# Optimization experiments

Hardware: AMD Instinct MI355X
Metric: run time of the kernel (lower is better)

The kernel has to match this reference:

```python
import jax, jax.numpy as jnp
import numpy as np
from jax import lax

CH = 16      # channel_n
HID = 128    # hidden_n
WDIM = 128   # w_dim


def _sobel_weight():
    sx = np.array([[-1, 0, 1], [-2, 0, 2], [-1, 0, 1]], dtype=np.float32).reshape(1, 1, 3, 3)
    sy = np.array([[-1, -2, -1], [0, 0, 0], [1, 2, 1]], dtype=np.float32).reshape(1, 1, 3, 3)
    sx = np.repeat(sx, CH, axis=0)  # [16,1,3,3]
    sy = np.repeat(sy, CH, axis=0)  # [16,1,3,3]
    return jnp.asarray(np.concatenate([sx, sy], axis=0))  # [32,1,3,3] torch grouped-conv OIHW layout


def setup_inputs() -> dict:
    key = jax.random.key(0)
    k1, k2, k3, k4 = jax.random.split(key, 4)
    B, H, W = 8, 96, 96
    x = jax.random.uniform(k1, (B, CH, H, W), dtype=jnp.float32)
    w = jax.random.normal(k2, (B, WDIM), dtype=jnp.float32)
    sobel = _sobel_weight()
    # update_net params. NOTE: original fills W2 with 0.0 (trivial delta); we use
    W1 = jax.random.normal(k3, (HID, 3 * CH + WDIM), dtype=jnp.float32) * 0.05
    b1 = jnp.zeros((HID,), dtype=jnp.float32)
    W2 = jax.random.normal(k4, (CH, HID), dtype=jnp.float32) * 0.02
    return {"x": x, "w": w, "sobel": sobel, "W1": W1, "b1": b1, "W2": W2, "steps": 64}


def _living_mask(alpha):
    # max_pool2d(3, stride=1, pad=1) > 0.1 ; torch pads with -inf for max pool
    m = lax.reduce_window(alpha, -jnp.inf, lax.max, (1, 1, 3, 3), (1, 1, 1, 1), 'SAME')
    return m > 0.1


def reference(x, w, sobel, W1, b1, W2, steps):
    B, _, H, Wd = x.shape
    w_exp = jnp.broadcast_to(w[:, :, None, None], (B, WDIM, H, Wd))

    def step(xc, key):
        pre_life = _living_mask(xc[:, 3:4])
        perception = lax.conv_general_dilated(
            xc, sobel, (1, 1), 'SAME', feature_group_count=CH,
            dimension_numbers=('NCHW', 'OIHW', 'NCHW'))  # [B,32,H,W]
        comb = jnp.concatenate([xc, perception, w_exp], axis=1)  # [B,176,H,W]
        h = jax.nn.relu(jnp.einsum('bchw,nc->bnhw', comb, W1) + b1[None, :, None, None])
        delta = jnp.einsum('bnhw,cn->bchw', h, W2)
        alpha = xc[:, 3:4]
        upd = (jax.random.uniform(key, alpha.shape) < 0.5) & (alpha > 0.1)
        xn = xc + delta * upd.astype(xc.dtype)
        life = pre_life & _living_mask(xn[:, 3:4])
        xn = xn * life.astype(xn.dtype)
        return xn, None

    keys = jax.random.split(jax.random.key(42), steps)
    x_final, _ = lax.scan(step, x, keys)
    return x_final
```

## Files before the change

kernel.cpp:

```cpp
#include <hip/hip_runtime.h>
#include <stdint.h>


#define CHN 16
#define HIDN 128
#define WD 128
#define NB 8
#define NH 96
#define NW 96
#define NSTEPS 64
#define TW 16
#define TH 4
#define PLANE (NH*NW)
#define TILES_X (NW/TW)
#define TILES_Y (NH/TH)
#define TPI (TILES_X*TILES_Y)
#define NBLK (NB*TPI)
#define HW_ (TH+2)
#define WW_ (TW+2)
#define NF4 (HW_*WW_*4)
#define NT 256

typedef float v2f __attribute__((ext_vector_type(2)));

__host__ __device__ __forceinline__ uint32_t rotl(uint32_t v, int d){ return (v<<d)|(v>>(32-d)); }

__host__ __device__ __forceinline__ void threefry2x32(uint32_t k0, uint32_t k1,
                                                      uint32_t x0, uint32_t x1,
                                                      uint32_t &o0, uint32_t &o1){
  uint32_t k2 = k0 ^ k1 ^ 0x1BD11BDAu;
  x0 += k0; x1 += k1;
  x0 += x1; x1 = rotl(x1,13); x1 ^= x0;
  x0 += x1; x1 = rotl(x1,15); x1 ^= x0;
  x0 += x1; x1 = rotl(x1,26); x1 ^= x0;
  x0 += x1; x1 = rotl(x1, 6); x1 ^= x0;
  x0 += k1; x1 += k2 + 1u;
  x0 += x1; x1 = rotl(x1,17); x1 ^= x0;
  x0 += x1; x1 = rotl(x1,29); x1 ^= x0;
  x0 += x1; x1 = rotl(x1,16); x1 ^= x0;
  x0 += x1; x1 = rotl(x1,24); x1 ^= x0;
  x0 += k2; x1 += k0 + 2u;
  x0 += x1; x1 = rotl(x1,13); x1 ^= x0;
  x0 += x1; x1 = rotl(x1,15); x1 ^= x0;
  x0 += x1; x1 = rotl(x1,26); x1 ^= x0;
  x0 += x1; x1 = rotl(x1, 6); x1 ^= x0;
  x0 += k0; x1 += k1 + 3u;
  x0 += x1; x1 = rotl(x1,17); x1 ^= x0;
  x0 += x1; x1 = rotl(x1,29); x1 ^= x0;
  x0 += x1; x1 = rotl(x1,16); x1 ^= x0;
  x0 += x1; x1 = rotl(x1,24); x1 ^= x0;
  x0 += k1; x1 += k2 + 4u;
  x0 += x1; x1 = rotl(x1,13); x1 ^= x0;
  x0 += x1; x1 = rotl(x1,15); x1 ^= x0;
  x0 += x1; x1 = rotl(x1,26); x1 ^= x0;
  x0 += x1; x1 = rotl(x1, 6); x1 ^= x0;
  x0 += k2; x1 += k0 + 5u;
  o0 = x0; o1 = x1;
}

__global__ __launch_bounds__(256) void nca_pre(
    const float* __restrict__ w, const float* __restrict__ W1,
    const float* __restrict__ b1, const float* __restrict__ W2,
    float* __restrict__ w1eff, float* __restrict__ w2t, float* __restrict__ c1)
{
  const int b = blockIdx.x, t = threadIdx.x;
  if (b == 0){
    for (int idx = t; idx < HIDN*32; idx += 256){
      int n = idx >> 5, k = idx & 31;
      float v;
      if (k < 16) v = W1[n*176 + k];
      else { int cc = k - 16; v = W1[n*176 + 16 + 2*cc] + W1[n*176 + 17 + 2*cc]; }
      w1eff[idx] = v;
    }
    for (int idx = t; idx < HIDN*CHN; idx += 256){
      int n = idx >> 4, cc = idx & 15;
      w2t[idx] = W2[cc*HIDN + n];
    }
  }
  if (t < HIDN){
    float s = b1[t];
    const float* wrow = W1 + t*176 + 48;
    const float* wb = w + b*WD;
    #pragma unroll 8
    for (int k = 0; k < WD; ++k) s = fmaf(wrow[k], wb[k], s);
    c1[b*HIDN + t] = s;
  }
}

template<bool FIRST>
__global__ __launch_bounds__(NT, 4) void nca_step(
    const float* __restrict__ Xin,
    const unsigned char* __restrict__ Mp,
    const float* __restrict__ w1eff, const float* __restrict__ w2t,
    const float* __restrict__ c1,
    uint32_t key0, uint32_t key1,
    float* __restrict__ Yn, unsigned char* __restrict__ Mn)
{
  __shared__ float xs[HW_][WW_][20];
  __shared__ float ya[TH+4][TW+4];
  __shared__ float lifes[HW_][WW_];
  __shared__ float ufs[64];
  __shared__ float red[4][CHN][64];

  const int T = blockIdx.x;
  const int b = T & 7;
  const int t = T >> 3;
  const int tw0 = (t % TILES_X)*TW, th0 = (t / TILES_X)*TH;
  const int tid = threadIdx.x;

  if (FIRST){
    for (int idx = tid; idx < CHN*HW_*WW_; idx += NT){
      int ch = idx / (HW_*WW_), rem = idx % (HW_*WW_);
      int hh = rem / WW_, ww = rem % WW_;
      int g2 = th0 - 1 + hh, w2 = tw0 - 1 + ww;
      float v = 0.f;
      if ((unsigned)g2 < NH && (unsigned)w2 < NW)
        v = Xin[((b*CHN + ch)*NH + g2)*NW + w2];
      xs[hh][ww][ch] = v;
    }
  } else {
    if (tid < (TH+4)*(TW+4)){
      int hh = tid / (TW+4), ww = tid % (TW+4);
      int g2 = th0 - 2 + hh, w2 = tw0 - 2 + ww;
      float v = 0.f;
      if ((unsigned)g2 < NH && (unsigned)w2 < NW)
        v = Xin[(size_t)(b*PLANE + g2*NW + w2)*CHN + 3];
      ya[hh][ww] = v;
    }
    float4 xr[2];
    #pragma unroll
    for (int i = 0; i < 2; ++i){
      int idx = tid + i*NT;
      float4 v = make_float4(0.f,0.f,0.f,0.f);
      if (idx < NF4){
        int hh = idx / (WW_*4);
        int rem = idx % (WW_*4);
        int ww = rem >> 2, k4 = rem & 3;
        int g2 = th0 - 1 + hh, w2 = tw0 - 1 + ww;
        if ((unsigned)g2 < NH && (unsigned)w2 < NW)
          v = *(const float4*)(Xin + (size_t)(b*PLANE + g2*NW + w2)*CHN + k4*4);
      }
      xr[i] = v;
    }
    __syncthreads();
    if (tid < HW_*WW_){
      int hh = tid / WW_, ww = tid % WW_;
      int g2 = th0 - 1 + hh, w2 = tw0 - 1 + ww;
      float lf = 0.f;
      if ((unsigned)g2 < NH && (unsigned)w2 < NW){
        float mx = ya[hh][ww];
        #pragma unroll
        for (int dr = 0; dr < 3; ++dr)
          #pragma unroll
          for (int dc = 0; dc < 3; ++dc)
            mx = fmaxf(mx, ya[hh+dr][ww+dc]);
        lf = (Mp[b*PLANE + g2*NW + w2] && (mx > 0.1f)) ? 1.f : 0.f;
      }
      lifes[hh][ww] = lf;
    }
    __syncthreads();
    #pragma unroll
    for (int i = 0; i < 2; ++i){
      int idx = tid + i*NT;
      if (idx < NF4){
        int hh = idx / (WW_*4);
        int rem = idx % (WW_*4);
        int ww = rem >> 2, k4 = rem & 3;
        float lf = lifes[hh][ww];
        float4 v = xr[i];
        v.x *= lf; v.y *= lf; v.z *= lf; v.w *= lf;
        *(float4*)&xs[hh][ww][k4*4] = v;
      }
    }
  }
  __syncthreads();

  const int px = tid & 63;
  const int q  = tid >> 6;
  const int c = px & 15, r = px >> 4;
  const int gh = th0 + r, gw = tw0 + c;
  const int pos = b*PLANE + gh*NW + gw;

  #define LD4(dr,dc,k4) (*(const float4*)&xs[r+(dr)][c+(dc)][(k4)*4])
  const v2f two = (v2f){2.f, 2.f};
  float4 xc4[4];
  v2f xp[8], pp[8];
  #pragma unroll
  for (int k4 = 0; k4 < 4; ++k4){
    xc4[k4] = LD4(1,1,k4);
    xp[2*k4]   = (v2f){xc4[k4].x, xc4[k4].y};
    xp[2*k4+1] = (v2f){xc4[k4].z, xc4[k4].w};
  }
  #pragma unroll
  for (int k4 = 0; k4 < 2; ++k4){
    float4 a = LD4(0,2,k4), b0 = LD4(0,0,k4);
    float4 d = LD4(1,2,k4), e = LD4(1,0,k4);
    float4 f = LD4(2,2,k4), g = LD4(2,0,k4);
    v2f a0 = (v2f){a.x,a.y}, a1 = (v2f){a.z,a.w};
    v2f b0v= (v2f){b0.x,b0.y},b1v= (v2f){b0.z,b0.w};
    v2f d0 = (v2f){d.x,d.y}, d1 = (v2f){d.z,d.w};
    v2f e0 = (v2f){e.x,e.y}, e1 = (v2f){e.z,e.w};
    v2f f0 = (v2f){f.x,f.y}, f1 = (v2f){f.z,f.w};
    v2f g0 = (v2f){g.x,g.y}, g1 = (v2f){g.z,g.w};
    pp[2*k4]   = (a0-b0v) + two*(d0-e0) + (f0-g0);
    pp[2*k4+1] = (a1-b1v) + two*(d1-e1) + (f1-g1);
  }
  #pragma unroll
  for (int k4 = 2; k4 < 4; ++k4){
    float4 a = LD4(2,0,k4), b0 = LD4(0,0,k4);
    float4 d = LD4(2,1,k4), e = LD4(0,1,k4);
    float4 f = LD4(2,2,k4), g = LD4(0,2,k4);
    v2f a0 = (v2f){a.x,a.y}, a1 = (v2f){a.z,a.w};
    v2f b0v= (v2f){b0.x,b0.y},b1v= (v2f){b0.z,b0.w};
    v2f d0 = (v2f){d.x,d.y}, d1 = (v2f){d.z,d.w};
    v2f e0 = (v2f){e.x,e.y}, e1 = (v2f){e.z,e.w};
    v2f f0 = (v2f){f.x,f.y}, f1 = (v2f){f.z,f.w};
    v2f g0 = (v2f){g.x,g.y}, g1 = (v2f){g.z,g.w};
    pp[2*k4]   = (a0-b0v) + two*(d0-e0) + (f0-g0);
    pp[2*k4+1] = (a1-b1v) + two*(d1-e1) + (f1-g1);
  }
  #undef LD4

  if (q == 0){
    uint32_t o0, o1;
    threefry2x32(key0, key1, 0u, (uint32_t)pos, o0, o1);
    ufs[px] = ((((o0 ^ o1) >> 31) == 0u) && (xc4[0].w > 0.1f)) ? 1.f : 0.f;
  } else if (q == 1){
    float mx = xs[r][c][3];
    #pragma unroll
    for (int dr = 0; dr < 3; ++dr)
      #pragma unroll
      for (int dc = 0; dc < 3; ++dc)
        mx = fmaxf(mx, xs[r+dr][c+dc][3]);
    Mn[pos] = (mx > 0.1f) ? (unsigned char)1 : (unsigned char)0;
  }

  v2f acc2[8];
  #pragma unroll
  for (int i = 0; i < 8; ++i) acc2[i] = (v2f){0.f, 0.f};
  const int nbase = __builtin_amdgcn_readfirstlane(q) << 5;
  const float* c1b = c1 + b*HIDN;

  #pragma unroll 4
  for (int nn = 0; nn < 32; ++nn){
    const int n = nbase + nn;
    const v2f* wx = (const v2f*)(w1eff + (n << 5));
    v2f h01 = (v2f){c1b[n], 0.f};
    v2f h23 = (v2f){0.f, 0.f};
    #pragma unroll
    for (int k = 0; k < 8; ++k){
      h01 = __builtin_elementwise_fma(xp[k], wx[k],   h01);
      h23 = __builtin_elementwise_fma(pp[k], wx[8+k], h23);
    }
    float hv = fmaxf((h01.x + h01.y) + (h23.x + h23.y), 0.f);
    v2f hvv = (v2f){hv, hv};
    const v2f* w2p = (const v2f*)(w2t + (n << 4));
    #pragma unroll
    for (int cc2 = 0; cc2 < 8; ++cc2)
      acc2[cc2] = __builtin_elementwise_fma(hvv, w2p[cc2], acc2[cc2]);
  }

  #pragma unroll
  for (int cc2 = 0; cc2 < 8; ++cc2){
    red[q][2*cc2  ][px] = acc2[cc2].x;
    red[q][2*cc2+1][px] = acc2[cc2].y;
  }
  __syncthreads();

  {
    float uf = ufs[px];
    int ch = q << 2;
    float v0 = ((red[0][ch+0][px] + red[1][ch+0][px]) + (red[2][ch+0][px] + red[3][ch+0][px]));
    float v1 = ((red[0][ch+1][px] + red[1][ch+1][px]) + (red[2][ch+1][px] + red[3][ch+1][px]));
    float v2 = ((red[0][ch+2][px] + red[1][ch+2][px]) + (red[2][ch+2][px] + red[3][ch+2][px]));
    float v3 = ((red[0][ch+3][px] + red[1][ch+3][px]) + (red[2][ch+3][px] + red[3][ch+3][px]));
    float4 o = make_float4(fmaf(v0, uf, xc4[q].x), fmaf(v1, uf, xc4[q].y),
                           fmaf(v2, uf, xc4[q].z), fmaf(v3, uf, xc4[q].w));
    *(float4*)(Yn + (size_t)pos*CHN + q*4) = o;
  }
}

__global__ __launch_bounds__(256) void nca_final(
    const float* __restrict__ Yp, const unsigned char* __restrict__ Mp,
    float* __restrict__ out)
{
  __shared__ float ya[TH+4][TW+4];
  __shared__ float lifes[TH][TW];
  const int T = blockIdx.x;
  const int b = T & 7;
  const int t = T >> 3;
  const int tw0 = (t % TILES_X)*TW, th0 = (t / TILES_X)*TH;
  const int tid = threadIdx.x;
  if (tid < (TH+4)*(TW+4)){
    int hh = tid / (TW+4), ww = tid % (TW+4);
    int g2 = th0 - 2 + hh, w2 = tw0 - 2 + ww;
    float v = 0.f;
    if ((unsigned)g2 < NH && (unsigned)w2 < NW)
      v = Yp[(size_t)(b*PLANE + g2*NW + w2)*CHN + 3];
    ya[hh][ww] = v;
  }
  __syncthreads();
  if (tid < TH*TW){
    int i = tid >> 4, j = tid & 15;
    float mx = ya[i+2][j+2];
    #pragma unroll
    for (int dr = 0; dr < 3; ++dr)
      #pragma unroll
      for (int dc = 0; dc < 3; ++dc)
        mx = fmaxf(mx, ya[i+1+dr][j+1+dc]);
    lifes[i][j] = (Mp[b*PLANE + (th0+i)*NW + (tw0+j)] && (mx > 0.1f)) ? 1.f : 0.f;
  }
  __syncthreads();
  for (int idx = tid; idx < CHN*TH*TW; idx += 256){
    int ch = idx >> 6, p = idx & 63;
    int i = p >> 4, j = p & 15;
    int pos = b*PLANE + (th0+i)*NW + (tw0+j);
    out[((b*CHN + ch)*NH + th0 + i)*NW + tw0 + j] = Yp[(size_t)pos*CHN + ch] * lifes[i][j];
  }
}

extern "C" void kernel_launch(void* const* d_in, const int* in_sizes, int n_in,
                              void* d_out, int out_size, void* d_ws, size_t ws_size,
                              hipStream_t stream) {
  const float* x  = (const float*)d_in[0];
  const float* w  = (const float*)d_in[1];
  const float* W1 = (const float*)d_in[3];
  const float* b1 = (const float*)d_in[4];
  const float* W2 = (const float*)d_in[5];
  float* out = (float*)d_out;
  char* ws = (char*)d_ws;

  size_t off = 0;
  float*    w1eff = (float*)(ws + off);    off += (size_t)HIDN*32*4;
  float*    w2t   = (float*)(ws + off);    off += (size_t)HIDN*CHN*4;
  float*    c1    = (float*)(ws + off);    off += (size_t)NB*HIDN*4;
  float*    Yb0   = (float*)(ws + off);    off += (size_t)NB*CHN*PLANE*4;
  float*    Yb1   = (float*)(ws + off);    off += (size_t)NB*CHN*PLANE*4;
  unsigned char* Mb0 = (unsigned char*)(ws + off); off += (size_t)NB*PLANE;
  unsigned char* Mb1 = (unsigned char*)(ws + off); off += (size_t)NB*PLANE;
  (void)ws_size; (void)in_sizes; (void)n_in; (void)out_size;

  uint32_t k0[NSTEPS], k1[NSTEPS];
  for (int s = 0; s < NSTEPS; ++s) threefry2x32(0u, 42u, 0u, (uint32_t)s, k0[s], k1[s]);

  nca_pre<<<dim3(NB), dim3(256), 0, stream>>>(w, W1, b1, W2, w1eff, w2t, c1);

  nca_step<true><<<dim3(NBLK), dim3(NT), 0, stream>>>(
      x, Mb1 , w1eff, w2t, c1, k0[0], k1[0], Yb0, Mb0);
  for (int s = 1; s < NSTEPS; ++s){
    const float* Yp = (s & 1) ? Yb0 : Yb1;
    float*       Yn = (s & 1) ? Yb1 : Yb0;
    const unsigned char* Mq = (s & 1) ? Mb0 : Mb1;
    unsigned char*       Mn = (s & 1) ? Mb1 : Mb0;
    nca_step<false><<<dim3(NBLK), dim3(NT), 0, stream>>>(
        Yp, Mq, w1eff, w2t, c1, k0[s], k1[s], Yn, Mn);
  }
  nca_final<<<dim3(NBLK), dim3(256), 0, stream>>>(Yb1, Mb1, out);
}
```

Measured before the change: 1.391 ms.

## Double tile height so each thread computes two pixels sharing weight loads

```diff
diff --git a/kernel.cpp b/kernel.cpp
--- a/kernel.cpp
+++ b/kernel.cpp
@@ -10,7 +10,7 @@
 #define NW 96
 #define NSTEPS 64
 #define TW 16
-#define TH 4
+#define TH 8
 #define PLANE (NH*NW)
 #define TILES_X (NW/TW)
 #define TILES_Y (NH/TH)
@@ -87,8 +87,49 @@
   }
 }
 
+__device__ __forceinline__ void perceive_nhwc(const float xs[HW_][WW_][20],
+                                              int r, int c, v2f* xp, v2f* pp){
+  #define LD4(dr,dc,k4) (*(const float4*)&xs[r+(dr)][c+(dc)][(k4)*4])
+  const v2f two = (v2f){2.f, 2.f};
+  #pragma unroll
+  for (int k4 = 0; k4 < 4; ++k4){
+    float4 v = LD4(1,1,k4);
+    xp[2*k4]   = (v2f){v.x, v.y};
+    xp[2*k4+1] = (v2f){v.z, v.w};
+  }
+  #pragma unroll
+  for (int k4 = 0; k4 < 2; ++k4){
+    float4 a = LD4(0,2,k4), b0 = LD4(0,0,k4);
+    float4 d = LD4(1,2,k4), e = LD4(1,0,k4);
+    float4 f = LD4(2,2,k4), g = LD4(2,0,k4);
+    v2f a0 = (v2f){a.x,a.y}, a1 = (v2f){a.z,a.w};
+    v2f b0v= (v2f){b0.x,b0.y},b1v= (v2f){b0.z,b0.w};
+    v2f d0 = (v2f){d.x,d.y}, d1 = (v2f){d.z,d.w};
+    v2f e0 = (v2f){e.x,e.y}, e1 = (v2f){e.z,e.w};
+    v2f f0 = (v2f){f.x,f.y}, f1 = (v2f){f.z,f.w};
+    v2f g0 = (v2f){g.x,g.y}, g1 = (v2f){g.z,g.w};
+    pp[2*k4]   = (a0-b0v) + two*(d0-e0) + (f0-g0);
+    pp[2*k4+1] = (a1-b1v) + two*(d1-e1) + (f1-g1);
+  }
+  #pragma unroll
+  for (int k4 = 2; k4 < 4; ++k4){
+    float4 a = LD4(2,0,k4), b0 = LD4(0,0,k4);
+    float4 d = LD4(2,1,k4), e = LD4(0,1,k4);
+    float4 f = LD4(2,2,k4), g = LD4(0,2,k4);
+    v2f a0 = (v2f){a.x,a.y}, a1 = (v2f){a.z,a.w};
+    v2f b0v= (v2f){b0.x,b0.y},b1v= (v2f){b0.z,b0.w};
+    v2f d0 = (v2f){d.x,d.y}, d1 = (v2f){d.z,d.w};
+    v2f e0 = (v2f){e.x,e.y}, e1 = (v2f){e.z,e.w};
+    v2f f0 = (v2f){f.x,f.y}, f1 = (v2f){f.z,f.w};
+    v2f g0 = (v2f){g.x,g.y}, g1 = (v2f){g.z,g.w};
+    pp[2*k4]   = (a0-b0v) + two*(d0-e0) + (f0-g0);
+    pp[2*k4+1] = (a1-b1v) + two*(d1-e1) + (f1-g1);
+  }
+  #undef LD4
+}
+
 template<bool FIRST>
-__global__ __launch_bounds__(NT, 4) void nca_step(
+__global__ __launch_bounds__(NT, 3) void nca_step(
     const float* __restrict__ Xin,
     const unsigned char* __restrict__ Mp,
     const float* __restrict__ w1eff, const float* __restrict__ w2t,
@@ -99,8 +140,8 @@
   __shared__ float xs[HW_][WW_][20];
   __shared__ float ya[TH+4][TW+4];
   __shared__ float lifes[HW_][WW_];
-  __shared__ float ufs[64];
-  __shared__ float red[4][CHN][64];
+  __shared__ float ufs[128];
+  __shared__ float red[4][CHN][128];
 
   const int T = blockIdx.x;
   const int b = T & 7;
@@ -127,9 +168,9 @@
         v = Xin[(size_t)(b*PLANE + g2*NW + w2)*CHN + 3];
       ya[hh][ww] = v;
     }
-    float4 xr[2];
-    #pragma unroll
-    for (int i = 0; i < 2; ++i){
+    float4 xr[3];
+    #pragma unroll
+    for (int i = 0; i < 3; ++i){
       int idx = tid + i*NT;
       float4 v = make_float4(0.f,0.f,0.f,0.f);
       if (idx < NF4){
@@ -160,7 +201,7 @@
     }
     __syncthreads();
     #pragma unroll
-    for (int i = 0; i < 2; ++i){
+    for (int i = 0; i < 3; ++i){
       int idx = tid + i*NT;
       if (idx < NF4){
         int hh = idx / (WW_*4);
@@ -177,67 +218,44 @@
 
   const int px = tid & 63;
   const int q  = tid >> 6;
-  const int c = px & 15, r = px >> 4;
-  const int gh = th0 + r, gw = tw0 + c;
-  const int pos = b*PLANE + gh*NW + gw;
-
-  #define LD4(dr,dc,k4) (*(const float4*)&xs[r+(dr)][c+(dc)][(k4)*4])
-  const v2f two = (v2f){2.f, 2.f};
-  float4 xc4[4];
-  v2f xp[8], pp[8];
-  #pragma unroll
-  for (int k4 = 0; k4 < 4; ++k4){
-    xc4[k4] = LD4(1,1,k4);
-    xp[2*k4]   = (v2f){xc4[k4].x, xc4[k4].y};
-    xp[2*k4+1] = (v2f){xc4[k4].z, xc4[k4].w};
-  }
-  #pragma unroll
-  for (int k4 = 0; k4 < 2; ++k4){
-    float4 a = LD4(0,2,k4), b0 = LD4(0,0,k4);
-    float4 d = LD4(1,2,k4), e = LD4(1,0,k4);
-    float4 f = LD4(2,2,k4), g = LD4(2,0,k4);
-    v2f a0 = (v2f){a.x,a.y}, a1 = (v2f){a.z,a.w};
-    v2f b0v= (v2f){b0.x,b0.y},b1v= (v2f){b0.z,b0.w};
-    v2f d0 = (v2f){d.x,d.y}, d1 = (v2f){d.z,d.w};
-    v2f e0 = (v2f){e.x,e.y}, e1 = (v2f){e.z,e.w};
-    v2f f0 = (v2f){f.x,f.y}, f1 = (v2f){f.z,f.w};
-    v2f g0 = (v2f){g.x,g.y}, g1 = (v2f){g.z,g.w};
-    pp[2*k4]   = (a0-b0v) + two*(d0-e0) + (f0-g0);
-    pp[2*k4+1] = (a1-b1v) + two*(d1-e1) + (f1-g1);
-  }
-  #pragma unroll
-  for (int k4 = 2; k4 < 4; ++k4){
-    float4 a = LD4(2,0,k4), b0 = LD4(0,0,k4);
-    float4 d = LD4(2,1,k4), e = LD4(0,1,k4);
-    float4 f = LD4(2,2,k4), g = LD4(0,2,k4);
-    v2f a0 = (v2f){a.x,a.y}, a1 = (v2f){a.z,a.w};
-    v2f b0v= (v2f){b0.x,b0.y},b1v= (v2f){b0.z,b0.w};
-    v2f d0 = (v2f){d.x,d.y}, d1 = (v2f){d.z,d.w};
-    v2f e0 = (v2f){e.x,e.y}, e1 = (v2f){e.z,e.w};
-    v2f f0 = (v2f){f.x,f.y}, f1 = (v2f){f.z,f.w};
-    v2f g0 = (v2f){g.x,g.y}, g1 = (v2f){g.z,g.w};
-    pp[2*k4]   = (a0-b0v) + two*(d0-e0) + (f0-g0);
-    pp[2*k4+1] = (a1-b1v) + two*(d1-e1) + (f1-g1);
-  }
-  #undef LD4
+  const int c = px & 15, rr = px >> 4;
+  const int gh0 = th0 + rr, gh1 = gh0 + 4, gw = tw0 + c;
+  const int pos0 = b*PLANE + gh0*NW + gw;
+  const int pos1 = pos0 + 4*NW;
+
+  v2f xpA[8], ppA[8], xpB[8], ppB[8];
+  perceive_nhwc(xs, rr,   c, xpA, ppA);
+  perceive_nhwc(xs, rr+4, c, xpB, ppB);
 
   if (q == 0){
     uint32_t o0, o1;
-    threefry2x32(key0, key1, 0u, (uint32_t)pos, o0, o1);
-    ufs[px] = ((((o0 ^ o1) >> 31) == 0u) && (xc4[0].w > 0.1f)) ? 1.f : 0.f;
+    threefry2x32(key0, key1, 0u, (uint32_t)pos0, o0, o1);
+    ufs[px] = ((((o0 ^ o1) >> 31) == 0u) && (xpA[1].y > 0.1f)) ? 1.f : 0.f;
   } else if (q == 1){
-    float mx = xs[r][c][3];
+    uint32_t o0, o1;
+    threefry2x32(key0, key1, 0u, (uint32_t)pos1, o0, o1);
+    ufs[64 + px] = ((((o0 ^ o1) >> 31) == 0u) && (xpB[1].y > 0.1f)) ? 1.f : 0.f;
+  } else if (q == 2){
+    float mx = xs[rr][c][3];
     #pragma unroll
     for (int dr = 0; dr < 3; ++dr)
       #pragma unroll
       for (int dc = 0; dc < 3; ++dc)
-        mx = fmaxf(mx, xs[r+dr][c+dc][3]);
-    Mn[pos] = (mx > 0.1f) ? (unsigned char)1 : (unsigned char)0;
-  }
-
-  v2f acc2[8];
-  #pragma unroll
-  for (int i = 0; i < 8; ++i) acc2[i] = (v2f){0.f, 0.f};
+        mx = fmaxf(mx, xs[rr+dr][c+dc][3]);
+    Mn[pos0] = (mx > 0.1f) ? (unsigned char)1 : (unsigned char)0;
+  } else {
+    float mx = xs[rr+4][c][3];
+    #pragma unroll
+    for (int dr = 0; dr < 3; ++dr)
+      #pragma unroll
+      for (int dc = 0; dc < 3; ++dc)
+        mx = fmaxf(mx, xs[rr+4+dr][c+dc][3]);
+    Mn[pos1] = (mx > 0.1f) ? (unsigned char)1 : (unsigned char)0;
+  }
+
+  v2f accA[8], accB[8];
+  #pragma unroll
+  for (int i = 0; i < 8; ++i){ accA[i] = (v2f){0.f,0.f}; accB[i] = (v2f){0.f,0.f}; }
   const int nbase = __builtin_amdgcn_readfirstlane(q) << 5;
   const float* c1b = c1 + b*HIDN;
 
@@ -245,38 +263,55 @@
   for (int nn = 0; nn < 32; ++nn){
     const int n = nbase + nn;
     const v2f* wx = (const v2f*)(w1eff + (n << 5));
-    v2f h01 = (v2f){c1b[n], 0.f};
-    v2f h23 = (v2f){0.f, 0.f};
+    float c1n = c1b[n];
+    v2f h01a = (v2f){c1n, 0.f}, h23a = (v2f){0.f, 0.f};
+    v2f h01b = (v2f){c1n, 0.f}, h23b = (v2f){0.f, 0.f};
     #pragma unroll
     for (int k = 0; k < 8; ++k){
-      h01 = __builtin_elementwise_fma(xp[k], wx[k],   h01);
-      h23 = __builtin_elementwise_fma(pp[k], wx[8+k], h23);
-    }
-    float hv = fmaxf((h01.x + h01.y) + (h23.x + h23.y), 0.f);
-    v2f hvv = (v2f){hv, hv};
+      v2f w1k = wx[k], wpk = wx[8+k];
+      h01a = __builtin_elementwise_fma(xpA[k], w1k, h01a);
+      h23a = __builtin_elementwise_fma(ppA[k], wpk, h23a);
+      h01b = __builtin_elementwise_fma(xpB[k], w1k, h01b);
+      h23b = __builtin_elementwise_fma(ppB[k], wpk, h23b);
+    }
+    float hva = fmaxf((h01a.x + h01a.y) + (h23a.x + h23a.y), 0.f);
+    float hvb = fmaxf((h01b.x + h01b.y) + (h23b.x + h23b.y), 0.f);
+    v2f hva2 = (v2f){hva, hva}, hvb2 = (v2f){hvb, hvb};
     const v2f* w2p = (const v2f*)(w2t + (n << 4));
     #pragma unroll
-    for (int cc2 = 0; cc2 < 8; ++cc2)
-      acc2[cc2] = __builtin_elementwise_fma(hvv, w2p[cc2], acc2[cc2]);
+    for (int cc2 = 0; cc2 < 8; ++cc2){
+      v2f wv = w2p[cc2];
+      accA[cc2] = __builtin_elementwise_fma(hva2, wv, accA[cc2]);
+      accB[cc2] = __builtin_elementwise_fma(hvb2, wv, accB[cc2]);
+    }
   }
 
   #pragma unroll
   for (int cc2 = 0; cc2 < 8; ++cc2){
-    red[q][2*cc2  ][px] = acc2[cc2].x;
-    red[q][2*cc2+1][px] = acc2[cc2].y;
+    red[q][2*cc2  ][px]      = accA[cc2].x;
+    red[q][2*cc2+1][px]      = accA[cc2].y;
+    red[q][2*cc2  ][64 + px] = accB[cc2].x;
+    red[q][2*cc2+1][64 + px] = accB[cc2].y;
   }
   __syncthreads();
 
   {
-    float uf = ufs[px];
+    float uf0 = ufs[px], uf1 = ufs[64 + px];
     int ch = q << 2;
-    float v0 = ((red[0][ch+0][px] + red[1][ch+0][px]) + (red[2][ch+0][px] + red[3][ch+0][px]));
-    float v1 = ((red[0][ch+1][px] + red[1][ch+1][px]) + (red[2][ch+1][px] + red[3][ch+1][px]));
-    float v2 = ((red[0][ch+2][px] + red[1][ch+2][px]) + (red[2][ch+2][px] + red[3][ch+2][px]));
-    float v3 = ((red[0][ch+3][px] + red[1][ch+3][px]) + (red[2][ch+3][px] + red[3][ch+3][px]));
-    float4 o = make_float4(fmaf(v0, uf, xc4[q].x), fmaf(v1, uf, xc4[q].y),
-                           fmaf(v2, uf, xc4[q].z), fmaf(v3, uf, xc4[q].w));
-    *(float4*)(Yn + (size_t)pos*CHN + q*4) = o;
+    float a0 = ((red[0][ch+0][px] + red[1][ch+0][px]) + (red[2][ch+0][px] + red[3][ch+0][px]));
+    float a1 = ((red[0][ch+1][px] + red[1][ch+1][px]) + (red[2][ch+1][px] + red[3][ch+1][px]));
+    float a2 = ((red[0][ch+2][px] + red[1][ch+2][px]) + (red[2][ch+2][px] + red[3][ch+2][px]));
+    float a3 = ((red[0][ch+3][px] + red[1][ch+3][px]) + (red[2][ch+3][px] + red[3][ch+3][px]));
+    float4 oA = make_float4(fmaf(a0, uf0, xpA[2*q].x), fmaf(a1, uf0, xpA[2*q].y),
+                            fmaf(a2, uf0, xpA[2*q+1].x), fmaf(a3, uf0, xpA[2*q+1].y));
+    *(float4*)(Yn + (size_t)pos0*CHN + q*4) = oA;
+    float b0 = ((red[0][ch+0][64+px] + red[1][ch+0][64+px]) + (red[2][ch+0][64+px] + red[3][ch+0][64+px]));
+    float b1 = ((red[0][ch+1][64+px] + red[1][ch+1][64+px]) + (red[2][ch+1][64+px] + red[3][ch+1][64+px]));
+    float b2 = ((red[0][ch+2][64+px] + red[1][ch+2][64+px]) + (red[2][ch+2][64+px] + red[3][ch+2][64+px]));
+    float b3 = ((red[0][ch+3][64+px] + red[1][ch+3][64+px]) + (red[2][ch+3][64+px] + red[3][ch+3][64+px]));
+    float4 oB = make_float4(fmaf(b0, uf1, xpB[2*q].x), fmaf(b1, uf1, xpB[2*q].y),
+                            fmaf(b2, uf1, xpB[2*q+1].x), fmaf(b3, uf1, xpB[2*q+1].y));
+    *(float4*)(Yn + (size_t)pos1*CHN + q*4) = oB;
   }
 }
 
@@ -312,7 +347,7 @@
   }
   __syncthreads();
   for (int idx = tid; idx < CHN*TH*TW; idx += 256){
-    int ch = idx >> 6, p = idx & 63;
+    int ch = idx >> 7, p = idx & 127;
     int i = p >> 4, j = p & 15;
     int pos = b*PLANE + (th0+i)*NW + (tw0+j);
     out[((b*CHN + ch)*NH + th0 + i)*NW + tw0 + j] = Yp[(size_t)pos*CHN + ch] * lifes[i][j];
```

Result: slower. 2.159 ms (+55.2%).
